# Performance work log

Hardware: AMD Instinct MI355X
Metric: run time of the kernel (lower is better)

Reference implementation:

```python
import jax, jax.numpy as jnp
import numpy as np

N = 16          # num_transforms
BS = 128        # batch_size
D = 4096        # encoder dim
C, H, W = 3, 64, 64
TEMP = 0.5      # hyperparams.temperature
LAM_H = 1.0     # hyperparams.h
EPS = 1e-8      # torch CosineSimilarity eps


def setup_inputs() -> dict:
    key = jax.random.key(0)
    k1, k2, k3 = jax.random.split(key, 3)
    return {
        "pic_set": jax.random.normal(k1, (N, BS, C, H, W), dtype=jnp.float32),
        "dec_pics": jax.random.normal(k2, (N, BS, C, H, W), dtype=jnp.float32),
        "h": jax.random.normal(k3, (N, BS, D), dtype=jnp.float32),
    }


def _pos_neg_indices(n, bs):
    # Static (numpy) index construction replicating the boolean masks.
    # Positives of row i: all j != i with j % bs == i % bs (sorted, row-major),
    # Negatives of row i: all j with j % bs != i % bs (sorted).
    k = n * bs
    i = np.arange(k)
    cols = (i % bs)[:, None] + np.arange(n)[None, :] * bs          # (K, N)
    pos_idx = cols[cols != i[:, None]].reshape(k, n - 1)            # (K, N-1)
    jj = np.arange(k)
    neg_mask = (jj[None, :] % bs) != (i[:, None] % bs)              # (K, K)
    neg_idx = np.broadcast_to(jj, (k, k))[neg_mask].reshape(k, k - n)  # (K, K-N)
    return jnp.asarray(pos_idx), jnp.asarray(neg_idx)


def _nt_xent(h):
    n, bs, d = h.shape
    k = n * bs
    s = h.reshape(k, d)
    # CosineSimilarity(dim=2) with eps clamp on norms
    nrm = jnp.maximum(jnp.linalg.norm(s, axis=1), EPS)
    sn = s / nrm[:, None]
    simmat = (sn @ sn.T) / TEMP                                     # (K, K)
    pos_idx, neg_idx = _pos_neg_indices(n, bs)
    pos = jnp.take_along_axis(simmat, pos_idx, axis=1)              # (K, N-1)
    neg = jnp.take_along_axis(simmat, neg_idx, axis=1)              # (K, K-N)
    # CrossEntropyLoss(reduction='sum') with label 0 on logits
    # [pos_{i,m}, neg_i] == sum of logsumexp - pos; logsumexp over concat
    # factors as logaddexp(lse(neg_i), pos_{i,m}).
    neg_lse = jax.scipy.special.logsumexp(neg, axis=1)              # (K,)
    loss = jnp.sum(jnp.logaddexp(neg_lse[:, None], pos) - pos)
    kpos = k * (n - 1)
    return loss / kpos


def reference(pic_set, dec_pics, h):
    n, bs = pic_set.shape[0], pic_set.shape[1]
    loss_h = _nt_xent(h)
    # dec_pics[(i+1) % N] cyclic offset, then flat MSE (mean reduction)
    offset = (np.arange(n) + 1) % n
    p = pic_set.reshape(n, bs, -1)
    dshift = dec_pics.reshape(n, bs, -1)[offset]
    loss_pairs = jnp.mean((p - dshift) ** 2)
    return loss_pairs + LAM_H * loss_h
```

## Files before the change

kernel.cpp:

```cpp
#include <hip/hip_runtime.h>
#include <hip/hip_bf16.h>
#include <math.h>

#define N_T   16
#define BSZ   128
#define DDIM  4096
#define KROWS (N_T * BSZ)
#define CHW   (3 * 64 * 64)
#define S_PIC (BSZ * CHW)
#define T_MSE (N_T * S_PIC)
#define KPOS  (KROWS * (N_T - 1))

typedef short  bf16x8 __attribute__((ext_vector_type(8)));
typedef float  f32x4  __attribute__((ext_vector_type(4)));

__device__ __forceinline__ float waveReduceSum(float v) {
    for (int off = 32; off > 0; off >>= 1) v += __shfl_down(v, off, 64);
    return v;
}
__device__ __forceinline__ float waveReduceMax(float v) {
    for (int off = 32; off > 0; off >>= 1) v = fmaxf(v, __shfl_down(v, off, 64));
    return v;
}
__device__ __forceinline__ float blockReduceSum(float v) {
    __shared__ float s[8];
    int lane = threadIdx.x & 63, wid = threadIdx.x >> 6;
    v = waveReduceSum(v);
    if (lane == 0) s[wid] = v;
    __syncthreads();
    int nw = (blockDim.x + 63) >> 6;
    v = (threadIdx.x < nw) ? s[threadIdx.x] : 0.0f;
    if (wid == 0) v = waveReduceSum(v);
    return v;
}
__device__ __forceinline__ float blockReduceMax(float v) {
    __shared__ float s[8];
    int lane = threadIdx.x & 63, wid = threadIdx.x >> 6;
    v = waveReduceMax(v);
    if (lane == 0) s[wid] = v;
    __syncthreads();
    int nw = (blockDim.x + 63) >> 6;
    v = (threadIdx.x < nw) ? s[threadIdx.x] : -INFINITY;
    if (wid == 0) v = waveReduceMax(v);
    return v;
}

__global__ void mse_kernel(const float* __restrict__ pic,
                           const float* __restrict__ dec,
                           float* __restrict__ acc) {
    const int total4 = T_MSE / 4;
    float sum = 0.0f;
    for (int t = blockIdx.x * blockDim.x + threadIdx.x; t < total4;
         t += gridDim.x * blockDim.x) {
        int base = t * 4;
        int n    = base / S_PIC;
        int rest = base - n * S_PIC;
        const float4 p = *(const float4*)(pic + base);
        const float4 d = *(const float4*)(dec + ((n + 1) & (N_T - 1)) * S_PIC + rest);
        float dx = p.x - d.x, dy = p.y - d.y, dz = p.z - d.z, dw = p.w - d.w;
        sum += dx * dx + dy * dy + dz * dz + dw * dw;
    }
    sum = blockReduceSum(sum);
    if (threadIdx.x == 0) atomicAdd(acc, sum);
}

__global__ void norm_kernel(const float* __restrict__ h,
                            __hip_bfloat16* __restrict__ hb) {
    const int row = blockIdx.x;
    const float* r = h + (size_t)row * DDIM;
    float ss = 0.0f;
    for (int k = threadIdx.x * 8; k < DDIM; k += blockDim.x * 8) {
        float4 v0 = *(const float4*)(r + k);
        float4 v1 = *(const float4*)(r + k + 4);
        ss += v0.x * v0.x + v0.y * v0.y + v0.z * v0.z + v0.w * v0.w;
        ss += v1.x * v1.x + v1.y * v1.y + v1.z * v1.z + v1.w * v1.w;
    }
    ss = blockReduceSum(ss);
    __shared__ float scale_s;
    if (threadIdx.x == 0) scale_s = 1.0f / fmaxf(sqrtf(ss), 1e-8f);
    __syncthreads();
    const float sc = scale_s;
    __hip_bfloat16* ob = hb + (size_t)row * DDIM;
    for (int k = threadIdx.x * 8; k < DDIM; k += blockDim.x * 8) {
        float4 v0 = *(const float4*)(r + k);
        float4 v1 = *(const float4*)(r + k + 4);
        __hip_bfloat16 t[8];
        t[0] = __float2bfloat16(v0.x * sc); t[1] = __float2bfloat16(v0.y * sc);
        t[2] = __float2bfloat16(v0.z * sc); t[3] = __float2bfloat16(v0.w * sc);
        t[4] = __float2bfloat16(v1.x * sc); t[5] = __float2bfloat16(v1.y * sc);
        t[6] = __float2bfloat16(v1.z * sc); t[7] = __float2bfloat16(v1.w * sc);
        *(bf16x8*)(ob + k) = *(const bf16x8*)t;
    }
}

__global__ __launch_bounds__(256) void gemm_mfma(const ushort* __restrict__ X,
                                                 float* __restrict__ C) {
    __shared__ ushort As[128 * 32];
    __shared__ ushort Bs[128 * 32];
    const int tid  = threadIdx.x;
    const int wave = tid >> 6, lane = tid & 63;
    const int wm = wave >> 1, wn = wave & 1;
    const int quad = lane >> 4, l16 = lane & 15;
    const int bi = blockIdx.y, bj = blockIdx.x;

    f32x4 acc[4][4];
#pragma unroll
    for (int i = 0; i < 4; i++)
#pragma unroll
        for (int j = 0; j < 4; j++) acc[i][j] = (f32x4){0.f, 0.f, 0.f, 0.f};

    const int srow = lane >> 2;
    const int scol = (lane & 3) * 8;
    const ushort* Ag0 = X + (size_t)(bi * 128 + wave * 16       + srow) * DDIM + scol;
    const ushort* Ag1 = X + (size_t)(bi * 128 + (wave + 4) * 16 + srow) * DDIM + scol;
    const ushort* Bg0 = X + (size_t)(bj * 128 + wave * 16       + srow) * DDIM + scol;
    const ushort* Bg1 = X + (size_t)(bj * 128 + (wave + 4) * 16 + srow) * DDIM + scol;
    ushort* Al0 = As + wave * 512;
    ushort* Al1 = As + (wave + 4) * 512;
    ushort* Bl0 = Bs + wave * 512;
    ushort* Bl1 = Bs + (wave + 4) * 512;

    for (int kk = 0; kk < DDIM; kk += 32) {
        __syncthreads();
        __builtin_amdgcn_global_load_lds(
            (const __attribute__((address_space(1))) unsigned int*)(Ag0 + kk),
            (__attribute__((address_space(3))) unsigned int*)Al0, 16, 0, 0);
        __builtin_amdgcn_global_load_lds(
            (const __attribute__((address_space(1))) unsigned int*)(Ag1 + kk),
            (__attribute__((address_space(3))) unsigned int*)Al1, 16, 0, 0);
        __builtin_amdgcn_global_load_lds(
            (const __attribute__((address_space(1))) unsigned int*)(Bg0 + kk),
            (__attribute__((address_space(3))) unsigned int*)Bl0, 16, 0, 0);
        __builtin_amdgcn_global_load_lds(
            (const __attribute__((address_space(1))) unsigned int*)(Bg1 + kk),
            (__attribute__((address_space(3))) unsigned int*)Bl1, 16, 0, 0);
        __syncthreads();

        bf16x8 a[4], b[4];
#pragma unroll
        for (int t = 0; t < 4; t++)
            a[t] = *(const bf16x8*)(As + (wm * 64 + t * 16 + l16) * 32 + quad * 8);
#pragma unroll
        for (int t = 0; t < 4; t++)
            b[t] = *(const bf16x8*)(Bs + (wn * 64 + t * 16 + l16) * 32 + quad * 8);
#pragma unroll
        for (int mt = 0; mt < 4; mt++)
#pragma unroll
            for (int nt = 0; nt < 4; nt++)
                acc[mt][nt] = __builtin_amdgcn_mfma_f32_16x16x32_bf16(
                    a[mt], b[nt], acc[mt][nt], 0, 0, 0);
    }

#pragma unroll
    for (int mt = 0; mt < 4; mt++) {
#pragma unroll
        for (int r = 0; r < 4; r++) {
            const int row = bi * 128 + wm * 64 + mt * 16 + quad * 4 + r;
            float* o = C + (size_t)row * KROWS + bj * 128 + wn * 64 + l16;
#pragma unroll
            for (int nt = 0; nt < 4; nt++) o[nt * 16] = 2.0f * acc[mt][nt][r];
        }
    }
}

__global__ void lse_kernel(const float* __restrict__ C, float* __restrict__ acc) {
    const int i = blockIdx.x;
    __shared__ float srow[KROWS];
    const float* row = C + (size_t)i * KROWS;
    for (int j = threadIdx.x; j < KROWS; j += blockDim.x) srow[j] = row[j];
    __syncthreads();

    const int ires = i & (BSZ - 1);
    float m = -INFINITY;
    for (int j = threadIdx.x; j < KROWS; j += blockDim.x)
        if ((j & (BSZ - 1)) != ires) m = fmaxf(m, srow[j]);
    m = blockReduceMax(m);
    __shared__ float mS;
    if (threadIdx.x == 0) mS = m;
    __syncthreads();
    m = mS;
    float se = 0.0f;
    for (int j = threadIdx.x; j < KROWS; j += blockDim.x)
        if ((j & (BSZ - 1)) != ires) se += expf(srow[j] - m);
    se = blockReduceSum(se);

    if (threadIdx.x == 0) {
        const float neg_lse = m + logf(se);
        float loss = 0.0f;
#pragma unroll
        for (int t = 0; t < N_T; t++) {
            const int j = ires + t * BSZ;
            if (j == i) continue;
            const float x = neg_lse - srow[j];
            loss += (x > 0.0f) ? (x + log1pf(expf(-x))) : log1pf(expf(x));
        }
        atomicAdd(acc + 1, loss);
    }
}

__global__ void finalize_kernel(const float* __restrict__ acc, float* __restrict__ out) {
    if (threadIdx.x == 0 && blockIdx.x == 0)
        out[0] = acc[0] / (float)T_MSE + acc[1] / (float)KPOS;
}

extern "C" void kernel_launch(void* const* d_in, const int* in_sizes, int n_in,
                              void* d_out, int out_size, void* d_ws, size_t ws_size,
                              hipStream_t stream) {
    const float* pic = (const float*)d_in[0];
    float* dec = (float*)d_in[1];
    const float* h = (const float*)d_in[2];
    float* out = (float*)d_out;

    float* acc = (float*)d_ws;
    const size_t hbuf_bytes   = (size_t)KROWS * DDIM * sizeof(__hip_bfloat16);
    const size_t simmat_bytes = (size_t)KROWS * KROWS * sizeof(float);
    __hip_bfloat16* hbuf;
    float* simmat;
    if (ws_size >= 256 + hbuf_bytes + simmat_bytes) {
        hbuf   = (__hip_bfloat16*)((char*)d_ws + 256);
        simmat = (float*)((char*)d_ws + 256 + hbuf_bytes);
    } else {
        hbuf   = (__hip_bfloat16*)dec;
        simmat = (float*)((char*)dec + hbuf_bytes);
    }

    hipMemsetAsync(d_ws, 0, 256, stream);
    mse_kernel<<<2048, 256, 0, stream>>>(pic, dec, acc);
    norm_kernel<<<KROWS, 256, 0, stream>>>(h, hbuf);
    dim3 ggrid(KROWS / 128, KROWS / 128);
    gemm_mfma<<<ggrid, 256, 0, stream>>>((const ushort*)hbuf, simmat);
    lse_kernel<<<KROWS, 256, 0, stream>>>(simmat, acc);
    finalize_kernel<<<1, 64, 0, stream>>>(acc, out);
}
```

Before: 360.2 us.

## Split GEMM K dimension across two partial buffers and restructure MSE grid

The similarity GEMM now launches a z-dimension of two, with each block handling half of the 4096-long reduction and writing to its own partial matrix. The LSE kernel sums the two partials while loading each row. This doubles the block count from 256 to 512 so all CUs on the device get work, at the cost of an extra 16 MB partial write and read. The MSE kernel is also rewritten to use a 2D grid with fixed per-thread unrolled loads and no per-element division.

```diff
diff --git a/kernel.cpp b/kernel.cpp
--- a/kernel.cpp
+++ b/kernel.cpp
@@ -45,21 +45,23 @@
     return v;
 }
 
-__global__ void mse_kernel(const float* __restrict__ pic,
-                           const float* __restrict__ dec,
-                           float* __restrict__ acc) {
-    const int total4 = T_MSE / 4;
-    float sum = 0.0f;
-    for (int t = blockIdx.x * blockDim.x + threadIdx.x; t < total4;
-         t += gridDim.x * blockDim.x) {
-        int base = t * 4;
-        int n    = base / S_PIC;
-        int rest = base - n * S_PIC;
-        const float4 p = *(const float4*)(pic + base);
-        const float4 d = *(const float4*)(dec + ((n + 1) & (N_T - 1)) * S_PIC + rest);
-        float dx = p.x - d.x, dy = p.y - d.y, dz = p.z - d.z, dw = p.w - d.w;
-        sum += dx * dx + dy * dy + dz * dz + dw * dw;
-    }
+__global__ __launch_bounds__(256) void mse_kernel(const float* __restrict__ pic,
+                                                  const float* __restrict__ dec,
+                                                  float* __restrict__ acc) {
+    const int n = blockIdx.y;
+    const size_t off = (size_t)n * S_PIC + (size_t)blockIdx.x * 8192 + threadIdx.x * 4;
+    const size_t doff = (size_t)(((n + 1) & (N_T - 1)) - n) * S_PIC;
+    const float* p = pic + off;
+    const float* d = dec + off + doff;
+    float s0 = 0.f, s1 = 0.f, s2 = 0.f, s3 = 0.f;
+#pragma unroll
+    for (int k = 0; k < 8; k++) {
+        float4 a = *(const float4*)(p + k * 1024);
+        float4 b = *(const float4*)(d + k * 1024);
+        float dx = a.x - b.x, dy = a.y - b.y, dz = a.z - b.z, dw = a.w - b.w;
+        s0 += dx * dx; s1 += dy * dy; s2 += dz * dz; s3 += dw * dw;
+    }
+    float sum = (s0 + s1) + (s2 + s3);
     sum = blockReduceSum(sum);
     if (threadIdx.x == 0) atomicAdd(acc, sum);
 }
@@ -94,7 +96,7 @@
 }
 
 __global__ __launch_bounds__(256) void gemm_mfma(const ushort* __restrict__ X,
-                                                 float* __restrict__ C) {
+                                                 float* __restrict__ Cpart) {
     __shared__ ushort As[128 * 32];
     __shared__ ushort Bs[128 * 32];
     const int tid  = threadIdx.x;
@@ -102,6 +104,7 @@
     const int wm = wave >> 1, wn = wave & 1;
     const int quad = lane >> 4, l16 = lane & 15;
     const int bi = blockIdx.y, bj = blockIdx.x;
+    const int kz = blockIdx.z;
 
     f32x4 acc[4][4];
 #pragma unroll
@@ -120,7 +123,8 @@
     ushort* Bl0 = Bs + wave * 512;
     ushort* Bl1 = Bs + (wave + 4) * 512;
 
-    for (int kk = 0; kk < DDIM; kk += 32) {
+    const int k0 = kz * (DDIM / 2), k1 = k0 + (DDIM / 2);
+    for (int kk = k0; kk < k1; kk += 32) {
         __syncthreads();
         __builtin_amdgcn_global_load_lds(
             (const __attribute__((address_space(1))) unsigned int*)(Ag0 + kk),
@@ -151,23 +155,25 @@
                     a[mt], b[nt], acc[mt][nt], 0, 0, 0);
     }
 
+    float* Cp = Cpart + (size_t)kz * KROWS * KROWS;
 #pragma unroll
     for (int mt = 0; mt < 4; mt++) {
 #pragma unroll
         for (int r = 0; r < 4; r++) {
             const int row = bi * 128 + wm * 64 + mt * 16 + quad * 4 + r;
-            float* o = C + (size_t)row * KROWS + bj * 128 + wn * 64 + l16;
+            float* o = Cp + (size_t)row * KROWS + bj * 128 + wn * 64 + l16;
 #pragma unroll
             for (int nt = 0; nt < 4; nt++) o[nt * 16] = 2.0f * acc[mt][nt][r];
         }
     }
 }
 
-__global__ void lse_kernel(const float* __restrict__ C, float* __restrict__ acc) {
+__global__ void lse_kernel(const float* __restrict__ Cpart, float* __restrict__ acc) {
     const int i = blockIdx.x;
     __shared__ float srow[KROWS];
-    const float* row = C + (size_t)i * KROWS;
-    for (int j = threadIdx.x; j < KROWS; j += blockDim.x) srow[j] = row[j];
+    const float* r0 = Cpart + (size_t)i * KROWS;
+    const float* r1 = r0 + (size_t)KROWS * KROWS;
+    for (int j = threadIdx.x; j < KROWS; j += blockDim.x) srow[j] = r0[j] + r1[j];
     __syncthreads();
 
     const int ires = i & (BSZ - 1);
@@ -213,7 +219,7 @@
 
     float* acc = (float*)d_ws;
     const size_t hbuf_bytes   = (size_t)KROWS * DDIM * sizeof(__hip_bfloat16);
-    const size_t simmat_bytes = (size_t)KROWS * KROWS * sizeof(float);
+    const size_t simmat_bytes = (size_t)2 * KROWS * KROWS * sizeof(float);
     __hip_bfloat16* hbuf;
     float* simmat;
     if (ws_size >= 256 + hbuf_bytes + simmat_bytes) {
@@ -225,9 +231,9 @@
     }
 
     hipMemsetAsync(d_ws, 0, 256, stream);
-    mse_kernel<<<2048, 256, 0, stream>>>(pic, dec, acc);
+    mse_kernel<<<dim3(192, N_T), 256, 0, stream>>>(pic, dec, acc);
     norm_kernel<<<KROWS, 256, 0, stream>>>(h, hbuf);
-    dim3 ggrid(KROWS / 128, KROWS / 128);
+    dim3 ggrid(KROWS / 128, KROWS / 128, 2);
     gemm_mfma<<<ggrid, 256, 0, stream>>>((const ushort*)hbuf, simmat);
     lse_kernel<<<KROWS, 256, 0, stream>>>(simmat, acc);
     finalize_kernel<<<1, 64, 0, stream>>>(acc, out);
```

Measured after the change: 328.7 us. -8.7%, faster.
